# Performance work log

Measured on AMD Instinct MI355X. Metric: run time of the kernel, lower is better.

## Reference

```python
import jax, jax.numpy as jnp
import numpy as np

B, S, H = 64, 256, 768


def _lstm_cell(x, h, c, Wih, Whh, b):
    # PyTorch LSTMCell gate order: i, f, g, o
    g = x @ Wih.T + h @ Whh.T + b
    i, f, gg, o = jnp.split(g, 4, axis=-1)
    c = jax.nn.sigmoid(f) * c + jax.nn.sigmoid(i) * jnp.tanh(gg)
    h = jax.nn.sigmoid(o) * jnp.tanh(c)
    return h, c


def _bilstm(x, Wih_f, Whh_f, b_f, Wih_b, Whh_b, b_b):
    Bb, Ss, D = x.shape
    Hh = Whh_f.shape[1]

    def scan_dir(xs, Wih, Whh, b):
        def step(carry, x_t):
            h, c = carry
            h, c = _lstm_cell(x_t, h, c, Wih, Whh, b)
            return (h, c), h
        init = (jnp.zeros((Bb, Hh), x.dtype), jnp.zeros((Bb, Hh), x.dtype))
        _, hs = jax.lax.scan(step, init, xs)
        return hs

    xt = jnp.swapaxes(x, 0, 1)                      # [S, B, D]
    hf = scan_dir(xt, Wih_f, Whh_f, b_f)            # [S, B, H]
    hb = scan_dir(xt[::-1], Wih_b, Whh_b, b_b)[::-1]
    return jnp.swapaxes(jnp.concatenate([hf, hb], -1), 0, 1)  # [B, S, 2H]


def _decode(lstm_out, golds, subw_Wih, subw_Whh, subw_b,
            word_Wih, word_Whh, word_b, cls_W, cls_b):
    Bb, Ss, D = lstm_out.shape
    Hh = subw_Whh.shape[1]
    bidx = jnp.arange(Bb)
    subw_map = jnp.array([1, 2, 2], dtype=jnp.int32)   # subword_action_map
    word_map = jnp.array([0, 1, 1], dtype=jnp.int32)   # word_action_map

    sh = jnp.zeros((Bb, 2 * Ss + 2, Hh), lstm_out.dtype)  # subword stack (h)
    sc = jnp.zeros((Bb, 2 * Ss + 2, Hh), lstm_out.dtype)  # subword stack (c)
    wh = jnp.zeros((Bb, Ss + 1, Hh), lstm_out.dtype)       # word stack (h)
    wc = jnp.zeros((Bb, Ss + 1, Hh), lstm_out.dtype)       # word stack (c)
    sp = jnp.zeros((Bb,), jnp.int32)
    wp = jnp.zeros((Bb,), jnp.int32)

    xt = jnp.swapaxes(lstm_out, 0, 1)  # [S, B, 2H]
    gt = jnp.swapaxes(golds, 0, 1).astype(jnp.int32)
    xs = (xt[:-1], xt[1:], gt[1:])     # idx = 1..S-1

    def step(carry, inputs):
        sh, sc, sp, wh, wc, wp = carry
        x_prev, x_cur, g = inputs
        # subword stack LSTM: read top, push new state at pos+1
        h1, c1 = _lstm_cell(x_prev, sh[bidx, sp], sc[bidx, sp], subw_Wih, subw_Whh, subw_b)
        sh = sh.at[bidx, sp + 1].set(h1)
        sc = sc.at[bidx, sp + 1].set(c1)
        subword = jnp.concatenate([h1, c1], axis=-1)   # [B, 2H]
        # word stack LSTM
        wh1, wc1 = _lstm_cell(subword, wh[bidx, wp], wc[bidx, wp], word_Wih, word_Whh, word_b)
        wh = wh.at[bidx, wp + 1].set(wh1)
        wc = wc.at[bidx, wp + 1].set(wc1)
        out = jnp.concatenate([wh1, x_cur], axis=-1) @ cls_W.T + cls_b  # [B, 2]
        # training path: pos updates driven by gold actions
        sp = sp + subw_map[g]
        wp = wp + word_map[g]
        return (sh, sc, sp, wh, wc, wp), out

    _, outs = jax.lax.scan(step, (sh, sc, sp, wh, wc, wp), xs)  # [S-1, B, 2]
    first = jnp.broadcast_to(jnp.array([-1.0, 1.0], lstm_out.dtype), (Bb, 1, 2))
    return jnp.concatenate([first, jnp.swapaxes(outs, 0, 1)], axis=1)  # [B, S, 2]


def setup_inputs() -> dict:
    key = jax.random.key(0)
    ks = jax.random.split(key, 16)
    w = lambda k, shp: jax.random.normal(k, shp, dtype=jnp.float32) * 0.02
    return {
        "hidden_state": jax.random.normal(ks[0], (B, S, H), dtype=jnp.float32),
        "golds": jax.random.randint(ks[1], (B, S), 0, 2, dtype=jnp.int32),
        "lstm_Wih_f": w(ks[2], (4 * H, H)),
        "lstm_Whh_f": w(ks[3], (4 * H, H)),
        "lstm_b_f": w(ks[4], (4 * H,)),
        "lstm_Wih_b": w(ks[5], (4 * H, H)),
        "lstm_Whh_b": w(ks[6], (4 * H, H)),
        "lstm_b_b": w(ks[7], (4 * H,)),
        "subw_Wih": w(ks[8], (4 * H, 2 * H)),
        "subw_Whh": w(ks[9], (4 * H, H)),
        "subw_b": w(ks[10], (4 * H,)),
        "word_Wih": w(ks[11], (4 * H, 2 * H)),
        "word_Whh": w(ks[12], (4 * H, H)),
        "word_b": w(ks[13], (4 * H,)),
        "cls_W": w(ks[14], (2, 3 * H)),
        "cls_b": w(ks[15], (2,)),
    }


def reference(hidden_state, lstm_Wih_f, lstm_Whh_f, lstm_b_f,
              lstm_Wih_b, lstm_Whh_b, lstm_b_b,
              subw_Wih, subw_Whh, subw_b,
              word_Wih, word_Whh, word_b,
              cls_W, cls_b, golds):
    lstm_out = _bilstm(hidden_state, lstm_Wih_f, lstm_Whh_f, lstm_b_f,
                       lstm_Wih_b, lstm_Whh_b, lstm_b_b)
    return _decode(lstm_out, golds, subw_Wih, subw_Whh, subw_b,
                   word_Wih, word_Whh, word_b, cls_W, cls_b)
```

## Files before the change

### kernel.cpp

```cpp
#include <hip/hip_runtime.h>

#define B_  64
#define S_  256
#define H_  768
#define H4_ 3072
#define D2_ 1536
#define SEG 64
#define USZ (64*2304)

using u16 = unsigned short;
using u32 = unsigned int;
using u64 = unsigned long long;
typedef __attribute__((ext_vector_type(8))) short bf16x8;
typedef __attribute__((ext_vector_type(4))) float f32x4;
typedef __attribute__((ext_vector_type(4))) unsigned int u32x4;

#define DEV __device__ __forceinline__

DEV float bf2f(u16 u){ union{u32 i; float f;} c; c.i = ((u32)u)<<16; return c.f; }
DEV u16 f2bf(float f){ union{float f; u32 i;} c; c.f = f; return (u16)((c.i + 0x7FFFu + ((c.i>>16)&1u)) >> 16); }
DEV float sigm(float x){ return 1.f/(1.f + __expf(-x)); }
DEV float tanh_(float x){ return 2.f/(1.f + __expf(-2.f*x)) - 1.f; }

DEV void astore32(u16* p, u32 v){ __hip_atomic_store((u32*)p, v, __ATOMIC_RELAXED, __HIP_MEMORY_SCOPE_AGENT); }
DEV int afload(const int* p){ return __hip_atomic_load(p, __ATOMIC_RELAXED, __HIP_MEMORY_SCOPE_AGENT); }

DEV f32x4 mfma16(bf16x8 a, bf16x8 b, f32x4 c){
  return __builtin_amdgcn_mfma_f32_16x16x32_bf16(a, b, c, 0, 0, 0);
}

DEV void llc_load96(const u16* p, u32x4& a0, u32x4& a1, u32x4& a2,
                    u32x4& a3, u32x4& a4, u32x4& a5){
  asm volatile(
    "global_load_dwordx4 %0, %6, off sc0 sc1\n\t"
    "global_load_dwordx4 %1, %6, off offset:16 sc0 sc1\n\t"
    "global_load_dwordx4 %2, %6, off offset:32 sc0 sc1\n\t"
    "global_load_dwordx4 %3, %6, off offset:48 sc0 sc1\n\t"
    "global_load_dwordx4 %4, %6, off offset:64 sc0 sc1\n\t"
    "global_load_dwordx4 %5, %6, off offset:80 sc0 sc1\n\t"
    "s_waitcnt vmcnt(0)"
    : "=&v"(a0), "=&v"(a1), "=&v"(a2), "=&v"(a3), "=&v"(a4), "=&v"(a5)
    : "v"(p));
}
DEV void stage48llc(u16* dst, const u16* src){
  u32x4 a0,a1,a2,a3,a4,a5;
  llc_load96(src, a0,a1,a2,a3,a4,a5);
  *(u32x4*)(dst)    = a0; *(u32x4*)(dst+8)  = a1;
  *(u32x4*)(dst+16) = a2; *(u32x4*)(dst+24) = a3;
  *(u32x4*)(dst+32) = a4; *(u32x4*)(dst+40) = a5;
}
DEV void stage48llcz(u16* dst, const u16* src, bool keep){
  u32x4 a0,a1,a2,a3,a4,a5;
  llc_load96(src, a0,a1,a2,a3,a4,a5);
  const u32x4 z = {0u,0u,0u,0u};
  if (!keep){ a0=z; a1=z; a2=z; a3=z; a4=z; a5=z; }
  *(u32x4*)(dst)    = a0; *(u32x4*)(dst+8)  = a1;
  *(u32x4*)(dst+16) = a2; *(u32x4*)(dst+24) = a3;
  *(u32x4*)(dst+32) = a4; *(u32x4*)(dst+40) = a5;
}

__global__ void k_conv(const float* __restrict__ src, u16* __restrict__ dst,
                       int cols, int sld, int dld){
  const long r = blockIdx.x;
  for (int c = threadIdx.x*4; c < cols; c += 1024) {
    const float* sp = src + r*sld + c;
    float a = sp[0], b = sp[1], cc = sp[2], d = sp[3];
    u64 pack = (u64)f2bf(a) | ((u64)f2bf(b)<<16) | ((u64)f2bf(cc)<<32) | ((u64)f2bf(d)<<48);
    *(u64*)(dst + r*dld + c) = pack;
  }
}

__global__ __launch_bounds__(256) void k_gemm(
    const u16* __restrict__ A, const u16* __restrict__ W,
    const float* __restrict__ bias, u16* __restrict__ C, int K, int t0)
{
  __shared__ u16 at[128*40];
  __shared__ u16 bt[128*40];
  const int tid = threadIdx.x;
  const int L = tid & 63, wv = tid >> 6;
  const int mq = wv >> 1, nq = wv & 1;
  const int l16 = L & 15, quad = L >> 4;
  const long mb = blockIdx.y, nb = blockIdx.x;

  f32x4 acc[4][4];
  #pragma unroll
  for (int m=0;m<4;++m)
    #pragma unroll
    for (int n=0;n<4;++n)
      acc[m][n] = (f32x4){0.f,0.f,0.f,0.f};

  const int r = tid >> 1, c0 = (tid & 1) * 16;
  const int fr = (int)mb*128 + r;
  const long arow = ((long)(fr >> 6))*S_ + t0 + (fr & 63);
  const u16* Arow = A + arow*(long)K + c0;
  const u16* Wrow = W + (nb*128 + r)*(long)K + c0;

  for (int kb = 0; kb < K; kb += 32) {
    *(u32x4*)&at[r*40 + c0]     = *(const u32x4*)(Arow + kb);
    *(u32x4*)&at[r*40 + c0 + 8] = *(const u32x4*)(Arow + kb + 8);
    *(u32x4*)&bt[r*40 + c0]     = *(const u32x4*)(Wrow + kb);
    *(u32x4*)&bt[r*40 + c0 + 8] = *(const u32x4*)(Wrow + kb + 8);
    __syncthreads();
    bf16x8 af[4], bfr[4];
    #pragma unroll
    for (int m=0;m<4;++m) af[m]  = *(const bf16x8*)&at[(mq*64 + m*16 + l16)*40 + quad*8];
    #pragma unroll
    for (int n=0;n<4;++n) bfr[n] = *(const bf16x8*)&bt[(nq*64 + n*16 + l16)*40 + quad*8];
    #pragma unroll
    for (int m=0;m<4;++m)
      #pragma unroll
      for (int n=0;n<4;++n)
        acc[m][n] = mfma16(af[m], bfr[n], acc[m][n]);
    __syncthreads();
  }
  #pragma unroll
  for (int n=0;n<4;++n) {
    const long col = nb*128 + nq*64 + n*16 + l16;
    const float bv = bias[col];
    #pragma unroll
    for (int m=0;m<4;++m) {
      const long row0 = mb*128 + mq*64 + m*16 + quad*4;
      #pragma unroll
      for (int rr=0;rr<4;++rr)
        C[(row0+rr)*3072 + col] = f2bf(acc[m][n][rr] + bv);
    }
  }
}

__global__ __launch_bounds__(512,2) void k_bilstm(
    const u16* __restrict__ Gf, const u16* __restrict__ Gb,
    const u16* __restrict__ Whhf, const u16* __restrict__ Whhb,
    const u16* __restrict__ h0, u16* __restrict__ lstm,
    float* __restrict__ cstf, float* __restrict__ cstb,
    int* __restrict__ flags, int t0f, int tb0, int ep0)
{
  __shared__ __align__(16) u16 lds[32*776];
  float* gbuf = (float*)lds;
  const int wg = blockIdx.x;
  const int dir = wg / 96, rem = wg % 96, mh = rem / 48, s = rem % 48;
  const int grp = dir*2 + mh;
  const int tid = threadIdx.x;
  const int wave = tid >> 6, q = wave & 3, kh = wave >> 2;
  const int L = tid & 63, l16 = L & 15, quad = L >> 4;
  const int srw = tid >> 4, scl = (tid & 15) * 48;

  const u16* Gsrc = dir ? Gb : Gf;
  const u16* W    = dir ? Whhb : Whhf;
  float* cst      = dir ? cstb : cstf;

  bf16x8 bfr[12];
  {
    const u16* wr = W + (long)(q*H_ + s*16 + l16)*H_ + kh*384 + quad*8;
    #pragma unroll
    for (int kk=0;kk<12;++kk) bfr[kk] = *(const bf16x8*)(wr + kk*32);
  }

  const int lb = tid >> 3, cdl = (tid & 7) * 2;
  const int eb = mh*32 + lb, col = s*16 + cdl;
  const bool ew = (tid < 256);
  float creg[2] = {0.f, 0.f};
  if (ew){ creg[0] = cst[eb*H_ + col]; creg[1] = cst[eb*H_ + col + 1]; }

  u32 g0=0,g1=0,g2=0,g3=0;
  if (ew){
    const int tp0 = dir ? (tb0 + SEG-1) : t0f;
    const int gidx = eb*SEG + (dir ? (tp0 - tb0) : (tp0 - t0f));
    const u16* grow = Gsrc + (long)gidx*H4_ + col;
    g0 = *(const u32*)(grow);      g1 = *(const u32*)(grow + H_);
    g2 = *(const u32*)(grow+2*H_); g3 = *(const u32*)(grow+3*H_);
  }

  for (int t=0; t<SEG; ++t) {
    const int tp = dir ? (tb0 + SEG-1 - t) : (t0f + t);
    const bool first = dir ? (tp == S_-1) : (tp == 0);
    const u16* hbase; long ldh;
    if (first){ hbase = h0 + dir*H_; ldh = D2_; }
    else {
      const int tprev = dir ? (tp+1) : (tp-1);
      hbase = lstm + (long)tprev*D2_ + dir*H_;
      ldh = (long)S_*D2_;
    }
    stage48llc(&lds[srw*776 + scl], hbase + (long)(mh*32 + srw)*ldh + scl);
    __syncthreads();
    f32x4 acc[2];
    acc[0] = (f32x4){0.f,0.f,0.f,0.f}; acc[1] = acc[0];
    #pragma unroll
    for (int kk=0;kk<12;++kk)
      #pragma unroll
      for (int m=0;m<2;++m){
        bf16x8 a = *(const bf16x8*)&lds[(m*16+l16)*776 + kh*384 + kk*32 + quad*8];
        acc[m] = mfma16(a, bfr[kk], acc[m]);
      }
    __syncthreads();
    #pragma unroll
    for (int m=0;m<2;++m)
      #pragma unroll
      for (int rr=0;rr<4;++rr)
        gbuf[(q*2+kh)*512 + (m*16+quad*4+rr)*16 + l16] = acc[m][rr];
    __syncthreads();
    if (ew){
      u32 gr[4] = {g0,g1,g2,g3};
      u32 hp = 0;
      #pragma unroll
      for (int i=0;i<2;++i){
        float gv[4];
        #pragma unroll
        for (int qq=0;qq<4;++qq)
          gv[qq] = gbuf[(qq*2+0)*512 + lb*16 + cdl+i]
                 + gbuf[(qq*2+1)*512 + lb*16 + cdl+i]
                 + bf2f((u16)(gr[qq] >> (16*i)));
        const float c = sigm(gv[1])*creg[i] + sigm(gv[0])*tanh_(gv[2]);
        creg[i] = c;
        const float h = sigm(gv[3])*tanh_(c);
        hp |= ((u32)f2bf(h)) << (16*i);
      }
      astore32(lstm + ((long)eb*S_ + tp)*D2_ + dir*H_ + col, hp);
    }
    __threadfence_block();
    __syncthreads();
    if (tid == 0)
      __hip_atomic_store(&flags[(grp*48 + s)*64], ep0 + t + 1, __ATOMIC_RELAXED, __HIP_MEMORY_SCOPE_AGENT);
    if (ew){
      const int t2 = t + 1;
      const int tp2 = dir ? (tb0 + SEG-1 - t2) : (t0f + t2);
      const long gidx2 = (long)eb*SEG + (dir ? (tp2 - tb0) : (tp2 - t0f));
      const u16* grow2 = Gsrc + gidx2*H4_ + col;
      g0 = *(const u32*)(grow2);      g1 = *(const u32*)(grow2 + H_);
      g2 = *(const u32*)(grow2+2*H_); g3 = *(const u32*)(grow2+3*H_);
    }
    if ((int)tid < 48) {
      while (afload(&flags[(grp*48 + (int)tid)*64]) < ep0 + t + 1)
        __builtin_amdgcn_s_sleep(1);
    }
    __syncthreads();
  }
  if (ew){ cst[eb*H_ + col] = creg[0]; cst[eb*H_ + col + 1] = creg[1]; }
}

__global__ __launch_bounds__(512,1) void k_decode(
    const u16* __restrict__ Gsub, const u16* __restrict__ Wsub,
    const u16* __restrict__ Wwrd, const float* __restrict__ wbias,
    const float* __restrict__ clsW, const int* __restrict__ golds,
    u16* __restrict__ U,
    float* __restrict__ scS, float* __restrict__ wcS, float* __restrict__ whS,
    float* __restrict__ partials, int* __restrict__ flags, int r0)
{
  __shared__ __align__(16) u16 ab[2][32*392];
  float* gbuf = (float*)ab;
  const int wg = blockIdx.x;
  const int role = wg / 96, rem = wg % 96, mh = rem / 48, s = rem % 48;
  const int grp = role*2 + mh;
  const int tid = threadIdx.x;
  const int wave = tid >> 6, q = wave & 3, kh = wave >> 2;
  const int L = tid & 63, l16 = L & 15, quad = L >> 4;
  const int su = tid & 255, srw = su >> 3, scl = (su & 7) * 48;
  const int lb = tid >> 3, cdl = (tid & 7)*2;
  const int eb = mh*32 + lb, col = s*16 + cdl;
  const bool ew = (tid < 256);
  const int sb = mh*32 + srw;

  bf16x8 wfr[36];
  float st0[2] = {0.f,0.f}, st1[2] = {0.f,0.f}, st2[2] = {0.f,0.f};
  float wbv[4][2], clv[2][2];
  if (role == 0){
    const u16* wr = Wsub + (long)(q*H_ + s*16 + l16)*H_ + kh*384 + quad*8;
    #pragma unroll
    for (int kk=0;kk<12;++kk) wfr[kk] = *(const bf16x8*)(wr + kk*32);
    if (ew){ st0[0] = scS[eb*H_+col]; st0[1] = scS[eb*H_+col+1]; }
  } else {
    const u16* wr = Wwrd + (long)(q*H_ + s*16 + l16)*2304 + kh*384 + quad*8;
    #pragma unroll
    for (int cc=0;cc<3;++cc)
      #pragma unroll
      for (int kk=0;kk<12;++kk)
        wfr[cc*12+kk] = *(const bf16x8*)(wr + cc*768 + kk*32);
    if (ew){
      st1[0] = wcS[eb*H_+col]; st1[1] = wcS[eb*H_+col+1];
      st2[0] = whS[eb*H_+col]; st2[1] = whS[eb*H_+col+1];
      #pragma unroll
      for (int qq=0;qq<4;++qq){ wbv[qq][0]=wbias[qq*H_+col]; wbv[qq][1]=wbias[qq*H_+col+1]; }
      clv[0][0]=clsW[col]; clv[0][1]=clsW[col+1];
      clv[1][0]=clsW[2304+col]; clv[1][1]=clsW[2304+col+1];
    }
  }

  int stg_g = golds[sb*S_ + ((r0 < 255) ? r0 : 255)];

  for (int rr=0; rr<SEG; ++rr){
    const int r = r0 + rr;
    u32 g0=0,g1=0,g2=0,g3=0; int gld_e = 0, gld = 0;
    if (ew){
      if (role == 0 && r <= 254){
        gld_e = golds[eb*S_ + r + 1];
        const u16* grow = Gsub + ((long)eb*SEG + rr)*H4_ + col;
        g0 = *(const u32*)(grow);      g1 = *(const u32*)(grow + H_);
        g2 = *(const u32*)(grow+2*H_); g3 = *(const u32*)(grow+3*H_);
      } else if (role == 1 && r >= 1){
        gld = golds[eb*S_ + r];
      }
    }
    if (tid < 96){
      int idx, tgt;
      if (tid < 48){ idx = mh*48 + tid; tgt = r; }
      else { idx = (2+mh)*48 + (tid-48); tgt = (role==0) ? (r-2) : r; }
      while (afload(&flags[idx*64]) < tgt) __builtin_amdgcn_s_sleep(1);
    }
    __syncthreads();

    const u16* Uprev = U + ((r+3)&3)*(long)USZ;
    u16*       Ucur  = U + (r&3)*(long)USZ;

    if (role == 0){
      if (r <= 254){
        const bool keep_s = (r > 0) && (stg_g == 0);
        const u16* urow = Uprev + (long)sb*2304 + scl;
        if (kh == 0){
          stage48llcz(&ab[0][srw*392 + scl], urow, keep_s);
        }
        __syncthreads();
        f32x4 acc[2];
        acc[0] = (f32x4){0.f,0.f,0.f,0.f}; acc[1] = acc[0];
        if (kh == 0){
          #pragma unroll
          for (int kk=0;kk<12;++kk)
            #pragma unroll
            for (int m=0;m<2;++m){
              bf16x8 a = *(const bf16x8*)&ab[0][(m*16+l16)*392 + kk*32 + quad*8];
              acc[m] = mfma16(a, wfr[kk], acc[m]);
            }
        } else {
          stage48llcz(&ab[1][srw*392 + scl], urow + 384, keep_s);
        }
        __syncthreads();
        if (kh == 1){
          #pragma unroll
          for (int kk=0;kk<12;++kk)
            #pragma unroll
            for (int m=0;m<2;++m){
              bf16x8 a = *(const bf16x8*)&ab[1][(m*16+l16)*392 + kk*32 + quad*8];
              acc[m] = mfma16(a, wfr[kk], acc[m]);
            }
        }
        __syncthreads();
        stg_g = golds[sb*S_ + ((r+1 < 255) ? r+1 : 255)];
        #pragma unroll
        for (int m=0;m<2;++m)
          #pragma unroll
          for (int r4=0;r4<4;++r4)
            gbuf[(q*2+kh)*512 + (m*16+quad*4+r4)*16 + l16] = acc[m][r4];
        __syncthreads();
        if (ew){
          const bool keep = (gld_e == 0);
          u32 gr[4] = {g0,g1,g2,g3};
          u32 hp=0, cp=0;
          #pragma unroll
          for (int i=0;i<2;++i){
            float gv[4];
            #pragma unroll
            for (int qq=0;qq<4;++qq)
              gv[qq] = gbuf[(qq*2+0)*512 + lb*16 + cdl+i]
                     + gbuf[(qq*2+1)*512 + lb*16 + cdl+i]
                     + bf2f((u16)(gr[qq] >> (16*i)));
            const float c1 = sigm(gv[1])*st0[i] + sigm(gv[0])*tanh_(gv[2]);
            const float h1 = sigm(gv[3])*tanh_(c1);
            st0[i] = keep ? c1 : 0.f;
            hp |= ((u32)f2bf(h1)) << (16*i);
            cp |= ((u32)f2bf(c1)) << (16*i);
          }
          astore32(Ucur + (long)eb*2304 + col, hp);
          astore32(Ucur + (long)eb*2304 + H_ + col, cp);
        }
      }
    } else {
      if (r >= 1){
        const u16* urow = Uprev + (long)sb*2304;
        if (kh == 0){
          stage48llc(&ab[0][srw*392 + scl], urow + scl);
        }
        __syncthreads();
        f32x4 acc[2];
        acc[0] = (f32x4){0.f,0.f,0.f,0.f}; acc[1] = acc[0];
        #pragma unroll
        for (int p=0;p<6;++p){
          if ((p & 1) == kh){
            const int cc = p >> 1;
            #pragma unroll
            for (int kk=0;kk<12;++kk)
              #pragma unroll
              for (int m=0;m<2;++m){
                bf16x8 a = *(const bf16x8*)&ab[p&1][(m*16+l16)*392 + kk*32 + quad*8];
                acc[m] = mfma16(a, wfr[cc*12+kk], acc[m]);
              }
          } else if (p < 5){
            stage48llc(&ab[(p+1)&1][srw*392 + scl], urow + (p+1)*384 + scl);
          }
          __syncthreads();
        }
        #pragma unroll
        for (int m=0;m<2;++m)
          #pragma unroll
          for (int r4=0;r4<4;++r4)
            gbuf[(q*2+kh)*512 + (m*16+quad*4+r4)*16 + l16] = acc[m][r4];
        __syncthreads();
        if (ew){
          const bool keep = (gld == 0);
          const int tp = r - 1;
          float p0 = 0.f, p1 = 0.f;
          u32 wp = 0;
          #pragma unroll
          for (int i=0;i<2;++i){
            float gv[4];
            #pragma unroll
            for (int qq=0;qq<4;++qq)
              gv[qq] = gbuf[(qq*2+0)*512 + lb*16 + cdl+i]
                     + gbuf[(qq*2+1)*512 + lb*16 + cdl+i]
                     + wbv[qq][i];
            const float wc1 = sigm(gv[1])*st1[i] + sigm(gv[0])*tanh_(gv[2]);
            const float wh1 = sigm(gv[3])*tanh_(wc1);
            st1[i] = keep ? st1[i] : wc1;
            st2[i] = keep ? st2[i] : wh1;
            p0 += wh1 * clv[0][i];
            p1 += wh1 * clv[1][i];
            wp |= ((u32)f2bf(st2[i])) << (16*i);
          }
          astore32(Ucur + (long)eb*2304 + D2_ + col, wp);
          p0 += __shfl_xor(p0, 1); p0 += __shfl_xor(p0, 2); p0 += __shfl_xor(p0, 4);
          p1 += __shfl_xor(p1, 1); p1 += __shfl_xor(p1, 2); p1 += __shfl_xor(p1, 4);
          if ((tid & 7) == 0){
            float* pp = partials + ((long)(tp*48 + s)*64 + eb)*2;
            pp[0] = p0; pp[1] = p1;
          }
        }
      }
    }
    __threadfence_block();
    __syncthreads();
    if (tid == 0)
      __hip_atomic_store(&flags[(grp*48 + s)*64], r+1, __ATOMIC_RELAXED, __HIP_MEMORY_SCOPE_AGENT);
  }
  if (ew){
    if (role == 0){
      scS[eb*H_+col] = st0[0]; scS[eb*H_+col+1] = st0[1];
    } else {
      wcS[eb*H_+col] = st1[0]; wcS[eb*H_+col+1] = st1[1];
      whS[eb*H_+col] = st2[0]; whS[eb*H_+col+1] = st2[1];
    }
  }
}

__global__ __launch_bounds__(256) void k_cls(
    const u16* __restrict__ lstm, const float* __restrict__ partials,
    const float* __restrict__ clsW, const float* __restrict__ clsb,
    float* __restrict__ out)
{
  const int ts = blockIdx.x;
  const int b  = blockIdx.y;
  const int tid = threadIdx.x;
  if (ts == 0) {
    if (tid == 0) { out[(long)b*S_*2 + 0] = -1.f; out[(long)b*S_*2 + 1] = 1.f; }
    return;
  }
  const int t = ts - 1;
  float s0 = 0.f, s1 = 0.f;
  const u16* xr = lstm + ((long)b*S_ + ts)*D2_;
  for (int k = tid; k < D2_; k += 256) {
    const float xv = bf2f(xr[k]);
    s0 += xv * clsW[768 + k];
    s1 += xv * clsW[2304 + 768 + k];
  }
  if (tid < 48) {
    const float* pr = partials + ((long)(t*48 + tid)*64 + b)*2;
    s0 += pr[0]; s1 += pr[1];
  }
  __shared__ float r0[256], r1[256];
  r0[tid] = s0; r1[tid] = s1; __syncthreads();
  for (int off = 128; off > 0; off >>= 1) {
    if (tid < off) { r0[tid] += r0[tid+off]; r1[tid] += r1[tid+off]; }
    __syncthreads();
  }
  if (tid == 0) {
    out[((long)b*S_ + ts)*2 + 0] = r0[0] + clsb[0];
    out[((long)b*S_ + ts)*2 + 1] = r1[0] + clsb[1];
  }
}

extern "C" void kernel_launch(void* const* d_in, const int* in_sizes, int n_in,
                              void* d_out, int out_size, void* d_ws, size_t ws_size,
                              hipStream_t stream)
{
  (void)in_sizes; (void)n_in; (void)out_size; (void)ws_size;
  const float* x     = (const float*)d_in[0];
  const int*   golds = (const int*)d_in[1];
  const float* wihf  = (const float*)d_in[2];
  const float* whhf  = (const float*)d_in[3];
  const float* bfw   = (const float*)d_in[4];
  const float* wihb  = (const float*)d_in[5];
  const float* whhb  = (const float*)d_in[6];
  const float* bbw   = (const float*)d_in[7];
  const float* swih  = (const float*)d_in[8];
  const float* swhh  = (const float*)d_in[9];
  const float* sb    = (const float*)d_in[10];
  const float* wwih  = (const float*)d_in[11];
  const float* wwhh  = (const float*)d_in[12];
  const float* wb    = (const float*)d_in[13];
  const float* clsW  = (const float*)d_in[14];
  const float* clsb  = (const float*)d_in[15];
  float* out = (float*)d_out;

  char* base = (char*)d_ws;
  u16*   U    = (u16*)(base + 0);
  u16*   h0   = (u16*)(base + 0);
  int*   flg2 = (int*)(base + 1179648);
  int*   flg4 = (int*)(base + 1228800);
  float* cstf = (float*)(base + 1277952);
  float* cstb = (float*)(base + 1474560);
  float* scS  = (float*)(base + 1671168);
  float* wcS  = (float*)(base + 1867776);
  float* whS  = (float*)(base + 2064384);
  u16* xb     = (u16*)(base + 2260992);
  u16* wihf_b = (u16*)(base + 27426816);
  u16* whhf_b = (u16*)(base + 32145408);
  u16* wihb_b = (u16*)(base + 36864000);
  u16* whhb_b = (u16*)(base + 41582592);
  u16* swih_b = (u16*)(base + 46301184);
  u16* swhh_b = (u16*)(base + 55738368);
  u16* wwrd_b = (u16*)(base + 60456960);
  u16* Gfseg  = (u16*)(base + 74612736);
  u16* Gbseg  = (u16*)(base + 99778560);
  u16* lstm   = (u16*)(base + 124944384);
  u16* Gsubseg = Gfseg;
  float* prt   = (float*)Gbseg;

  hipMemsetAsync(d_ws, 0, 2260992, stream);

  k_conv<<<16384, 256, 0, stream>>>(x,    xb,     768,  768,  768);
  k_conv<<<3072,  256, 0, stream>>>(wihf, wihf_b, 768,  768,  768);
  k_conv<<<3072,  256, 0, stream>>>(whhf, whhf_b, 768,  768,  768);
  k_conv<<<3072,  256, 0, stream>>>(wihb, wihb_b, 768,  768,  768);
  k_conv<<<3072,  256, 0, stream>>>(whhb, whhb_b, 768,  768,  768);
  k_conv<<<3072,  256, 0, stream>>>(swih, swih_b, 1536, 1536, 1536);
  k_conv<<<3072,  256, 0, stream>>>(swhh, swhh_b, 768,  768,  768);
  k_conv<<<3072,  256, 0, stream>>>(wwih, wwrd_b,        1536, 1536, 2304);
  k_conv<<<3072,  256, 0, stream>>>(wwhh, wwrd_b + 1536, 768,  768,  2304);

  dim3 gg(24, 32);
  for (int sgi = 0; sgi < 4; ++sgi) {
    const int t0f = sgi*SEG;
    const int tb0 = (3 - sgi)*SEG;
    k_gemm<<<gg, 256, 0, stream>>>(xb, wihf_b, bfw, Gfseg, 768, t0f);
    k_gemm<<<gg, 256, 0, stream>>>(xb, wihb_b, bbw, Gbseg, 768, tb0);
    k_bilstm<<<192, 512, 0, stream>>>(Gfseg, Gbseg, whhf_b, whhb_b, h0, lstm,
                                      cstf, cstb, flg2, t0f, tb0, sgi*SEG);
  }

  for (int sgi = 0; sgi < 4; ++sgi) {
    const int r0 = sgi*SEG;
    k_gemm<<<gg, 256, 0, stream>>>(lstm, swih_b, sb, Gsubseg, 1536, r0);
    k_decode<<<192, 512, 0, stream>>>(Gsubseg, swhh_b, wwrd_b, wb, clsW, golds,
                                      U, scS, wcS, whS, prt, flg4, r0);
  }

  dim3 gc(256, 64);
  k_cls<<<gc, 256, 0, stream>>>(lstm, prt, clsW, clsb, out);
}
```

Measured before the change: 4.109 ms.

## Deepen decode U ring buffer and stage full row with all waves

```diff
diff --git a/kernel.cpp b/kernel.cpp
--- a/kernel.cpp
+++ b/kernel.cpp
@@ -254,10 +254,13 @@
   const int wave = tid >> 6, q = wave & 3, kh = wave >> 2;
   const int L = tid & 63, l16 = L & 15, quad = L >> 4;
   const int su = tid & 255, srw = su >> 3, scl = (su & 7) * 48;
+  const int srw0 = tid >> 4, scl0 = (tid & 15) * 48;
   const int lb = tid >> 3, cdl = (tid & 7)*2;
   const int eb = mh*32 + lb, col = s*16 + cdl;
   const bool ew = (tid < 256);
-  const int sb = mh*32 + srw;
+  const int sb  = mh*32 + srw;
+  const int sb0 = mh*32 + srw0;
+  u16* abf = &ab[0][0];
 
   bf16x8 wfr[36];
   float st0[2] = {0.f,0.f}, st1[2] = {0.f,0.f}, st2[2] = {0.f,0.f};
@@ -284,7 +287,7 @@
     }
   }
 
-  int stg_g = golds[sb*S_ + ((r0 < 255) ? r0 : 255)];
+  int stg_g = golds[sb0*S_ + ((r0 < 255) ? r0 : 255)];
 
   for (int rr=0; rr<SEG; ++rr){
     const int r = r0 + rr;
@@ -302,47 +305,30 @@
     if (tid < 96){
       int idx, tgt;
       if (tid < 48){ idx = mh*48 + tid; tgt = r; }
-      else { idx = (2+mh)*48 + (tid-48); tgt = (role==0) ? (r-2) : r; }
+      else { idx = (2+mh)*48 + (tid-48); tgt = (role==0) ? (r-6) : r; }
       while (afload(&flags[idx*64]) < tgt) __builtin_amdgcn_s_sleep(1);
     }
     __syncthreads();
 
-    const u16* Uprev = U + ((r+3)&3)*(long)USZ;
-    u16*       Ucur  = U + (r&3)*(long)USZ;
+    const u16* Uprev = U + ((r+7)&7)*(long)USZ;
+    u16*       Ucur  = U + (r&7)*(long)USZ;
 
     if (role == 0){
       if (r <= 254){
         const bool keep_s = (r > 0) && (stg_g == 0);
-        const u16* urow = Uprev + (long)sb*2304 + scl;
-        if (kh == 0){
-          stage48llcz(&ab[0][srw*392 + scl], urow, keep_s);
-        }
+        stage48llcz(&abf[srw0*776 + scl0], Uprev + (long)sb0*2304 + scl0, keep_s);
         __syncthreads();
         f32x4 acc[2];
         acc[0] = (f32x4){0.f,0.f,0.f,0.f}; acc[1] = acc[0];
-        if (kh == 0){
+        #pragma unroll
+        for (int kk=0;kk<12;++kk)
           #pragma unroll
-          for (int kk=0;kk<12;++kk)
-            #pragma unroll
-            for (int m=0;m<2;++m){
-              bf16x8 a = *(const bf16x8*)&ab[0][(m*16+l16)*392 + kk*32 + quad*8];
-              acc[m] = mfma16(a, wfr[kk], acc[m]);
-            }
-        } else {
-          stage48llcz(&ab[1][srw*392 + scl], urow + 384, keep_s);
-        }
+          for (int m=0;m<2;++m){
+            bf16x8 a = *(const bf16x8*)&abf[(m*16+l16)*776 + kh*384 + kk*32 + quad*8];
+            acc[m] = mfma16(a, wfr[kk], acc[m]);
+          }
         __syncthreads();
-        if (kh == 1){
-          #pragma unroll
-          for (int kk=0;kk<12;++kk)
-            #pragma unroll
-            for (int m=0;m<2;++m){
-              bf16x8 a = *(const bf16x8*)&ab[1][(m*16+l16)*392 + kk*32 + quad*8];
-              acc[m] = mfma16(a, wfr[kk], acc[m]);
-            }
-        }
-        __syncthreads();
-        stg_g = golds[sb*S_ + ((r+1 < 255) ? r+1 : 255)];
+        stg_g = golds[sb0*S_ + ((r+1 < 255) ? r+1 : 255)];
         #pragma unroll
         for (int m=0;m<2;++m)
           #pragma unroll
@@ -508,7 +494,6 @@
   float* out = (float*)d_out;
 
   char* base = (char*)d_ws;
-  u16*   U    = (u16*)(base + 0);
   u16*   h0   = (u16*)(base + 0);
   int*   flg2 = (int*)(base + 1179648);
   int*   flg4 = (int*)(base + 1228800);
@@ -530,6 +515,7 @@
   u16* lstm   = (u16*)(base + 124944384);
   u16* Gsubseg = Gfseg;
   float* prt   = (float*)Gbseg;
+  u16* U       = (u16*)(base + 99778560 + 8388608);
 
   hipMemsetAsync(d_ws, 0, 2260992, stream);
 
@@ -553,6 +539,8 @@
                                       cstf, cstb, flg2, t0f, tb0, sgi*SEG);
   }
 
+  hipMemsetAsync(U, 0, 8*USZ*2, stream);
+
   for (int sgi = 0; sgi < 4; ++sgi) {
     const int r0 = sgi*SEG;
     k_gemm<<<gg, 256, 0, stream>>>(lstm, swih_b, sb, Gsubseg, 1536, r0);
```

Result: no change. 4.159 ms (+1.2%).
